# Kernel tuning notes

Measured on AMD Instinct MI355X. Metric: run time of the kernel, lower is better.

Reference implementation:

```python
import jax, jax.numpy as jnp
import numpy as np

N_NODES = 100000
N_EDGES = 1600000
IN_DIM = 128
HID = 32
HEADS = 4
NEG_SLOPE = 0.2


def gat_conv(x, src, dst, W, att_src, att_dst, bias, n_nodes, heads, out_ch):
    # x: [N, Fin], W: [Fin, heads*out_ch], att_*: [heads, out_ch], bias: [heads*out_ch]
    h = (x @ W).reshape(n_nodes, heads, out_ch)            # [N, H, C]
    a_src = jnp.einsum('nhc,hc->nh', h, att_src)           # [N, H]
    a_dst = jnp.einsum('nhc,hc->nh', h, att_dst)           # [N, H]
    e = jax.nn.leaky_relu(a_src[src] + a_dst[dst], NEG_SLOPE)  # [E, H]
    # segment softmax over incoming edges of each target node
    e_max = jax.ops.segment_max(e, dst, num_segments=n_nodes)  # [N, H]
    ex = jnp.exp(e - e_max[dst])                               # [E, H]
    denom = jax.ops.segment_sum(ex, dst, num_segments=n_nodes)  # [N, H]
    alpha = ex / denom[dst]                                     # [E, H]
    msg = h[src] * alpha[:, :, None]                            # [E, H, C]
    out = jax.ops.segment_sum(msg, dst, num_segments=n_nodes)   # [N, H, C]
    return out.reshape(n_nodes, heads * out_ch) + bias


def setup_inputs() -> dict:
    key = jax.random.key(0)
    ks = jax.random.split(key, 10)
    x = jax.random.normal(ks[0], (N_NODES, IN_DIM), dtype=jnp.float32)
    edge_index = jax.random.randint(ks[1], (2, N_EDGES), 0, N_NODES, dtype=jnp.int64) if jax.config.jax_enable_x64 else jax.random.randint(ks[1], (2, N_EDGES), 0, N_NODES, dtype=jnp.int32)
    s = 0.1
    W1 = jax.random.normal(ks[2], (IN_DIM, HEADS * HID), dtype=jnp.float32) * s
    att_src1 = jax.random.normal(ks[3], (HEADS, HID), dtype=jnp.float32) * s
    att_dst1 = jax.random.normal(ks[4], (HEADS, HID), dtype=jnp.float32) * s
    b1 = jnp.zeros((HEADS * HID,), dtype=jnp.float32)
    W2 = jax.random.normal(ks[5], (HEADS * HID, HEADS * HID), dtype=jnp.float32) * s
    att_src2 = jax.random.normal(ks[6], (HEADS, HID), dtype=jnp.float32) * s
    att_dst2 = jax.random.normal(ks[7], (HEADS, HID), dtype=jnp.float32) * s
    b2 = jnp.zeros((HEADS * HID,), dtype=jnp.float32)
    return {"x": x, "edge_index": edge_index, "W1": W1, "att_src1": att_src1,
            "att_dst1": att_dst1, "b1": b1, "W2": W2, "att_src2": att_src2,
            "att_dst2": att_dst2, "b2": b2}


def reference(x, edge_index, W1, att_src1, att_dst1, b1, W2, att_src2, att_dst2, b2):
    src, dst = edge_index[0], edge_index[1]
    x1 = jax.nn.relu(gat_conv(x, src, dst, W1, att_src1, att_dst1, b1, N_NODES, HEADS, HID))
    x2 = jax.nn.relu(gat_conv(x1, src, dst, W2, att_src2, att_dst2, b2, N_NODES, HEADS, HID))
    # [N, heads*hid, 2]
    return jnp.concatenate([x1[:, :, None], x2[:, :, None]], axis=2)
```

## Files before the change

### kernel.cpp

```cpp
#include <hip/hip_runtime.h>

#define NN 100000
#define NE 1600000
#define GEMM_GRID 1563
#define NBUK 391
#define BCAP 5120
#define PA_BLOCKS 320
#define PA_EDGES 5000
#define K1_GRID (16 + PA_BLOCKS)
#define K2_GRID (NBUK + GEMM_GRID)
#define AG1_GRID 6250
#define AGG2_GRID 12500

typedef short bf16x8 __attribute__((ext_vector_type(8)));
typedef float f32x4 __attribute__((ext_vector_type(4)));
typedef unsigned int u32;
typedef u32 u32x4 __attribute__((ext_vector_type(4)));
typedef unsigned short u16;

__device__ inline u32 bf16r(float x) {
    u32 u = __float_as_uint(x);
    return (u + 0x7FFFu + ((u >> 16) & 1u)) >> 16;
}

__device__ inline void split_pack8(const float a[8], u32 hh[4], u32 ll[4]) {
#pragma unroll
    for (int j = 0; j < 4; ++j) {
        u32 u0 = __float_as_uint(a[2 * j]);
        u32 u1 = __float_as_uint(a[2 * j + 1]);
        float l0 = a[2 * j] - __uint_as_float(u0 & 0xFFFF0000u);
        float l1 = a[2 * j + 1] - __uint_as_float(u1 & 0xFFFF0000u);
        hh[j] = (u0 >> 16) | (u1 & 0xFFFF0000u);
        ll[j] = (__float_as_uint(l0) >> 16) | (__float_as_uint(l1) & 0xFFFF0000u);
    }
}

__device__ inline void wpack_body(int idx, const float* __restrict__ W,
                                  bf16x8* __restrict__ wpH, bf16x8* __restrict__ wpL) {
    if (idx >= 2048) return;
    int lane = idx & 63, tile = idx >> 6;
    int kc = tile >> 3, ct = tile & 7;
    int col = lane & 15, kq = lane >> 4;
    int kbase = kc * 32 + kq * 8;
    float a[8];
#pragma unroll
    for (int i = 0; i < 8; ++i)
        a[i] = W[(size_t)(kbase + i) * 128 + ct * 16 + col];
    u32 hh[4], ll[4];
    split_pack8(a, hh, ll);
    wpH[tile * 64 + lane] = __builtin_bit_cast(bf16x8, (u32x4){hh[0], hh[1], hh[2], hh[3]});
    wpL[tile * 64 + lane] = __builtin_bit_cast(bf16x8, (u32x4){ll[0], ll[1], ll[2], ll[3]});
}

__global__ __launch_bounds__(256) void k1(
    const float* __restrict__ W1, bf16x8* __restrict__ wpH1, bf16x8* __restrict__ wpL1,
    const float* __restrict__ W2, bf16x8* __restrict__ wpH2, bf16x8* __restrict__ wpL2,
    const int* __restrict__ dst, const int* __restrict__ src,
    int* __restrict__ gtail, u32* __restrict__ tmp) {
    const int b = blockIdx.x;
    if (b < 8) {
        wpack_body(b * 256 + threadIdx.x, W1, wpH1, wpL1);
        return;
    } else if (b < 16) {
        wpack_body((b - 8) * 256 + threadIdx.x, W2, wpH2, wpL2);
        return;
    }
    __shared__ int lhist[NBUK], lcur[NBUK];
    const int t = threadIdx.x;
    const int e0 = (b - 16) * PA_EDGES;
    const int e1 = e0 + PA_EDGES;
    for (int i = t; i < NBUK; i += 256) lhist[i] = 0;
    __syncthreads();
    for (int e = e0 + t; e < e1; e += 256)
        atomicAdd(&lhist[dst[e] >> 8], 1);
    __syncthreads();
    for (int i = t; i < NBUK; i += 256)
        if (lhist[i] > 0) lcur[i] = atomicAdd(&gtail[i], lhist[i]);
    __syncthreads();
    for (int e = e0 + t; e < e1; e += 256) {
        int d = dst[e];
        int bb = d >> 8;
        int p = atomicAdd(&lcur[bb], 1);
        tmp[(size_t)bb * BCAP + p] = ((u32)(d & 255) << 17) | (u32)src[e];
    }
}

__device__ inline void gemm_epilogue(f32x4 acc[8], int row0, int w, int col, int kq,
                                     const float* __restrict__ atts,
                                     const float* __restrict__ attd,
                                     u16* __restrict__ hb,
                                     float* __restrict__ a_src,
                                     float* __restrict__ a_dst) {
    float as0[4], as1[4], ad0[4], ad1[4];
#pragma unroll
    for (int q = 0; q < 4; ++q) {
        as0[q] = atts[q * 32 + col];
        as1[q] = atts[q * 32 + 16 + col];
        ad0[q] = attd[q * 32 + col];
        ad1[q] = attd[q * 32 + 16 + col];
    }
#pragma unroll
    for (int r = 0; r < 4; ++r) {
        int node = row0 + w * 16 + kq * 4 + r;
        float ps[4], pd[4];
#pragma unroll
        for (int q = 0; q < 4; ++q) {
            float d0 = acc[2 * q][r], d1 = acc[2 * q + 1][r];
            ps[q] = d0 * as0[q] + d1 * as1[q];
            pd[q] = d0 * ad0[q] + d1 * ad1[q];
        }
#pragma unroll
        for (int off = 1; off < 16; off <<= 1) {
#pragma unroll
            for (int q = 0; q < 4; ++q) {
                ps[q] += __shfl_xor(ps[q], off);
                pd[q] += __shfl_xor(pd[q], off);
            }
        }
        if (node < NN) {
#pragma unroll
            for (int ct = 0; ct < 8; ++ct)
                hb[(size_t)node * 128 + ct * 16 + col] = (u16)bf16r(acc[ct][r]);
            if (col < 4) {
                float vs = col == 0 ? ps[0] : col == 1 ? ps[1] : col == 2 ? ps[2] : ps[3];
                float vd = col == 0 ? pd[0] : col == 1 ? pd[1] : col == 2 ? pd[2] : pd[3];
                a_src[node * 4 + col] = vs;
                a_dst[node * 4 + col] = vd;
            }
        }
    }
}

__global__ __launch_bounds__(256) void k2(
    const float* __restrict__ x,
    const bf16x8* __restrict__ wpH, const bf16x8* __restrict__ wpL,
    const float* __restrict__ atts, const float* __restrict__ attd,
    u16* __restrict__ hb, float* __restrict__ a_src, float* __restrict__ a_dst,
    const int* __restrict__ gtail, const u32* __restrict__ tmp,
    int* __restrict__ row_ptr, int* __restrict__ src_sorted) {
    __shared__ u32 ldata[BCAP];
    __shared__ int lh[256];
    __shared__ int lsc[256];
    const int idx = blockIdx.x;
    const int t = threadIdx.x;
    if (idx < NBUK) {
        const int g = idx;
        const int n = gtail[g];
        int acc = 0;
        for (int i = t; i < g; i += 256) acc += gtail[i];
        lsc[t] = acc;
        __syncthreads();
        for (int off = 128; off > 0; off >>= 1) {
            if (t < off) lsc[t] += lsc[t + off];
            __syncthreads();
        }
        const int ebase = lsc[0];
        lh[t] = 0;
        __syncthreads();
        for (int i = t; i < n; i += 256) {
            u32 v = tmp[(size_t)g * BCAP + i];
            ldata[i] = v;
            atomicAdd(&lh[v >> 17], 1);
        }
        __syncthreads();
        int c = lh[t];
        lsc[t] = c;
        __syncthreads();
        for (int off = 1; off < 256; off <<= 1) {
            int xv = (t >= off) ? lsc[t - off] : 0;
            __syncthreads();
            lsc[t] += xv;
            __syncthreads();
        }
        int excl = (t == 0) ? 0 : lsc[t - 1];
        int base = ebase + excl;
        lh[t] = base;
        int node = (g << 8) + t;
        if (node < NN) row_ptr[node] = base;
        if (g == NBUK - 1 && t == 0) row_ptr[NN] = ebase + n;
        __syncthreads();
        for (int i = t; i < n; i += 256) {
            u32 v = ldata[i];
            int p = atomicAdd(&lh[v >> 17], 1);
            src_sorted[p] = (int)(v & 0x1FFFFu);
        }
        return;
    }
    const int row0 = (idx - NBUK) * 64;
    const int lane = t & 63;
    const int w = t >> 6;
    const int col = lane & 15, kq = lane >> 4;
    int node_a = row0 + w * 16 + col;
    if (node_a > NN - 1) node_a = NN - 1;
    const float* xrow = x + (size_t)node_a * 128 + kq * 8;
    float a[32];
#pragma unroll
    for (int kc = 0; kc < 4; ++kc) {
        *(float4*)&a[kc * 8 + 0] = *(const float4*)(xrow + kc * 32);
        *(float4*)&a[kc * 8 + 4] = *(const float4*)(xrow + kc * 32 + 4);
    }
    f32x4 acc[8];
#pragma unroll
    for (int ct = 0; ct < 8; ++ct) acc[ct] = (f32x4){0.f, 0.f, 0.f, 0.f};
#pragma unroll
    for (int kc = 0; kc < 4; ++kc) {
        u32 hh[4], ll[4];
        split_pack8(&a[kc * 8], hh, ll);
        bf16x8 ah = __builtin_bit_cast(bf16x8, (u32x4){hh[0], hh[1], hh[2], hh[3]});
        bf16x8 al = __builtin_bit_cast(bf16x8, (u32x4){ll[0], ll[1], ll[2], ll[3]});
#pragma unroll
        for (int ct = 0; ct < 8; ++ct) {
            bf16x8 bh = wpH[(kc * 8 + ct) * 64 + lane];
            bf16x8 bl = wpL[(kc * 8 + ct) * 64 + lane];
            acc[ct] = __builtin_amdgcn_mfma_f32_16x16x32_bf16(ah, bh, acc[ct], 0, 0, 0);
            acc[ct] = __builtin_amdgcn_mfma_f32_16x16x32_bf16(al, bh, acc[ct], 0, 0, 0);
            acc[ct] = __builtin_amdgcn_mfma_f32_16x16x32_bf16(ah, bl, acc[ct], 0, 0, 0);
        }
    }
    gemm_epilogue(acc, row0, w, col, kq, atts, attd, hb, a_src, a_dst);
}

__global__ __launch_bounds__(256) void k_ag1(
    const u32* __restrict__ hb,
    const float* __restrict__ a_src, const float* __restrict__ a_dst,
    const int* __restrict__ row_ptr, const int* __restrict__ src_sorted,
    const float* __restrict__ bias1,
    const bf16x8* __restrict__ wpH2, const bf16x8* __restrict__ wpL2,
    const float* __restrict__ atts2, const float* __restrict__ attd2,
    u32* __restrict__ x1b, u16* __restrict__ hb2,
    float* __restrict__ a_src2, float* __restrict__ a_dst2) {
    __shared__ __align__(16) u32 xs[4][16][68];
    const int t = threadIdx.x;
    const int lane = t & 63;
    const int wv = t >> 6;
    const int q = lane >> 4;
    const int es = lane & 15;
    const int hbase = lane & 48;
    const int node0 = blockIdx.x * 16 + wv * 4;
    const float bv0 = bias1[lane * 2], bv1 = bias1[lane * 2 + 1];
#pragma unroll 1
    for (int ni = 0; ni < 4; ++ni) {
        const int node = node0 + ni;
        const int e0 = row_ptr[node], e1 = row_ptr[node + 1];
        const int emax = e1 - 1;
        const float advh = a_dst[node * 4 + q];
        float den = 0.f, a0a = 0.f, a0b = 0.f, a1a = 0.f, a1b = 0.f;
        if (e1 > e0) {
            int eidx = e0 + es;
            if (eidx > emax) eidx = emax;
            int sv = src_sorted[eidx];
            float av = a_src[sv * 4 + q];
            for (int ec = e0; ec < e1; ec += 16) {
                int cnt = e1 - ec;
                cnt = cnt < 16 ? cnt : 16;
                int eidxn = ec + 16 + es;
                if (eidxn > emax) eidxn = emax;
                int svn = src_sorted[eidxn];
                float avn = a_src[svn * 4 + q];
                float lk = av + advh;
                lk = lk > 0.f ? lk : 0.2f * lk;
                float ex = (es < cnt) ? __expf(lk - 8.f) : 0.f;
                den += ex;
                if (cnt == 16) {
                    u32 wvv[16];
#pragma unroll
                    for (int u = 0; u < 16; ++u) {
                        int su = __builtin_amdgcn_readlane(sv, u);
                        wvv[u] = hb[((size_t)su << 6) + lane];
                    }
                    float exu[16];
#pragma unroll
                    for (int u = 0; u < 16; ++u) exu[u] = __shfl(ex, hbase | u);
#pragma unroll
                    for (int u = 0; u < 16; ++u) {
                        float h0 = __uint_as_float(wvv[u] << 16);
                        float h1 = __uint_as_float(wvv[u] & 0xFFFF0000u);
                        if (u & 1) { a0b = fmaf(exu[u], h0, a0b); a1b = fmaf(exu[u], h1, a1b); }
                        else       { a0a = fmaf(exu[u], h0, a0a); a1a = fmaf(exu[u], h1, a1a); }
                    }
                } else {
                    for (int u0 = 0; u0 < cnt; u0 += 4) {
                        u32 wvv[4];
                        float exu[4];
#pragma unroll
                        for (int j = 0; j < 4; ++j) {
                            int su = __builtin_amdgcn_readlane(sv, u0 + j);
                            wvv[j] = hb[((size_t)su << 6) + lane];
                        }
#pragma unroll
                        for (int j = 0; j < 4; ++j) exu[j] = __shfl(ex, hbase | (u0 + j));
#pragma unroll
                        for (int j = 0; j < 4; ++j) {
                            float h0 = __uint_as_float(wvv[j] << 16);
                            float h1 = __uint_as_float(wvv[j] & 0xFFFF0000u);
                            if (j & 1) { a0b = fmaf(exu[j], h0, a0b); a1b = fmaf(exu[j], h1, a1b); }
                            else       { a0a = fmaf(exu[j], h0, a0a); a1a = fmaf(exu[j], h1, a1a); }
                        }
                    }
                }
                sv = svn;
                av = avn;
            }
        }
        float a0 = a0a + a0b, a1 = a1a + a1b;
#pragma unroll
        for (int m = 1; m < 16; m <<= 1) den += __shfl_xor(den, m);
        float inv = den > 0.f ? 1.f / den : 0.f;
        float r0 = fmaxf(fmaf(a0, inv, bv0), 0.f);
        float r1 = fmaxf(fmaf(a1, inv, bv1), 0.f);
        u32 pair = bf16r(r0) | (bf16r(r1) << 16);
        x1b[node * 64 + lane] = pair;
        xs[wv][ni][lane] = pair;
    }
    asm volatile("s_waitcnt lgkmcnt(0)" ::: "memory");
    __builtin_amdgcn_sched_barrier(0);
    const int col = lane & 15, kq = lane >> 4;
    int4 aw[4];
#pragma unroll
    for (int kc = 0; kc < 4; ++kc)
        aw[kc] = *(const int4*)&xs[wv][col & 3][kc * 16 + kq * 4];
    f32x4 acc[8];
#pragma unroll
    for (int ct = 0; ct < 8; ++ct) acc[ct] = (f32x4){0.f, 0.f, 0.f, 0.f};
#pragma unroll
    for (int kc = 0; kc < 4; ++kc) {
        bf16x8 a = __builtin_bit_cast(bf16x8, aw[kc]);
#pragma unroll
        for (int ct = 0; ct < 8; ++ct) {
            acc[ct] = __builtin_amdgcn_mfma_f32_16x16x32_bf16(a, wpH2[(kc * 8 + ct) * 64 + lane], acc[ct], 0, 0, 0);
            acc[ct] = __builtin_amdgcn_mfma_f32_16x16x32_bf16(a, wpL2[(kc * 8 + ct) * 64 + lane], acc[ct], 0, 0, 0);
        }
    }
    float as0[4], as1[4], ad0[4], ad1[4];
#pragma unroll
    for (int qq = 0; qq < 4; ++qq) {
        as0[qq] = atts2[qq * 32 + col];
        as1[qq] = atts2[qq * 32 + 16 + col];
        ad0[qq] = attd2[qq * 32 + col];
        ad1[qq] = attd2[qq * 32 + 16 + col];
    }
#pragma unroll
    for (int r = 0; r < 4; ++r) {
        int node = node0 + r;
        float ps[4], pd[4];
#pragma unroll
        for (int qq = 0; qq < 4; ++qq) {
            float d0 = acc[2 * qq][r], d1 = acc[2 * qq + 1][r];
            ps[qq] = d0 * as0[qq] + d1 * as1[qq];
            pd[qq] = d0 * ad0[qq] + d1 * ad1[qq];
        }
#pragma unroll
        for (int off = 1; off < 16; off <<= 1) {
#pragma unroll
            for (int qq = 0; qq < 4; ++qq) {
                ps[qq] += __shfl_xor(ps[qq], off);
                pd[qq] += __shfl_xor(pd[qq], off);
            }
        }
        if (kq == 0) {
#pragma unroll
            for (int ct = 0; ct < 8; ++ct)
                hb2[(size_t)node * 128 + ct * 16 + col] = (u16)bf16r(acc[ct][r]);
            if (col < 4) {
                float vs = col == 0 ? ps[0] : col == 1 ? ps[1] : col == 2 ? ps[2] : ps[3];
                float vd = col == 0 ? pd[0] : col == 1 ? pd[1] : col == 2 ? pd[2] : pd[3];
                a_src2[node * 4 + col] = vs;
                a_dst2[node * 4 + col] = vd;
            }
        }
    }
}

__global__ __launch_bounds__(256, 4) void k_agg2(
    const u32* __restrict__ hb,
    const float* __restrict__ a_src, const float* __restrict__ a_dst,
    const int* __restrict__ row_ptr, const int* __restrict__ src_sorted,
    const float* __restrict__ bias,
    const u32* __restrict__ x1b, float* __restrict__ outp) {
    const int lane = threadIdx.x & 63;
    const int node0 = blockIdx.x * 8 + (threadIdx.x >> 6) * 2;
    const int q = lane >> 4;
    const int es = lane & 15;
    const int hbase = lane & 48;
#pragma unroll
    for (int ni = 0; ni < 2; ++ni) {
        const int node = node0 + ni;
        if (node >= NN) continue;
        const int e0 = row_ptr[node], e1 = row_ptr[node + 1];
        const int emax = e1 - 1;
        const float advh = a_dst[node * 4 + q];
        float den = 0.f, a0a = 0.f, a0b = 0.f, a1a = 0.f, a1b = 0.f;
        if (e1 > e0) {
            int eidx = e0 + es;
            if (eidx > emax) eidx = emax;
            int sv = src_sorted[eidx];
            float av = a_src[sv * 4 + q];
            for (int ec = e0; ec < e1; ec += 16) {
                int cnt = e1 - ec;
                cnt = cnt < 16 ? cnt : 16;
                int eidxn = ec + 16 + es;
                if (eidxn > emax) eidxn = emax;
                int svn = src_sorted[eidxn];
                float avn = a_src[svn * 4 + q];
                float lk = av + advh;
                lk = lk > 0.f ? lk : 0.2f * lk;
                float ex = (es < cnt) ? __expf(lk - 8.f) : 0.f;
                den += ex;
                if (cnt == 16) {
                    u32 wv[16];
#pragma unroll
                    for (int u = 0; u < 16; ++u) {
                        int su = __builtin_amdgcn_readlane(sv, u);
                        wv[u] = hb[((size_t)su << 6) + lane];
                    }
                    float exu[16];
#pragma unroll
                    for (int u = 0; u < 16; ++u) exu[u] = __shfl(ex, hbase | u);
#pragma unroll
                    for (int u = 0; u < 16; ++u) {
                        float h0 = __uint_as_float(wv[u] << 16);
                        float h1 = __uint_as_float(wv[u] & 0xFFFF0000u);
                        if (u & 1) { a0b = fmaf(exu[u], h0, a0b); a1b = fmaf(exu[u], h1, a1b); }
                        else       { a0a = fmaf(exu[u], h0, a0a); a1a = fmaf(exu[u], h1, a1a); }
                    }
                } else {
                    for (int u0 = 0; u0 < cnt; u0 += 4) {
                        u32 wv[4];
                        float exu[4];
#pragma unroll
                        for (int j = 0; j < 4; ++j) {
                            int su = __builtin_amdgcn_readlane(sv, u0 + j);
                            wv[j] = hb[((size_t)su << 6) + lane];
                        }
#pragma unroll
                        for (int j = 0; j < 4; ++j) exu[j] = __shfl(ex, hbase | (u0 + j));
#pragma unroll
                        for (int j = 0; j < 4; ++j) {
                            float h0 = __uint_as_float(wv[j] << 16);
                            float h1 = __uint_as_float(wv[j] & 0xFFFF0000u);
                            if (j & 1) { a0b = fmaf(exu[j], h0, a0b); a1b = fmaf(exu[j], h1, a1b); }
                            else       { a0a = fmaf(exu[j], h0, a0a); a1a = fmaf(exu[j], h1, a1a); }
                        }
                    }
                }
                sv = svn;
                av = avn;
            }
        }
        float a0 = a0a + a0b, a1 = a1a + a1b;
#pragma unroll
        for (int m = 1; m < 16; m <<= 1) den += __shfl_xor(den, m);
        float inv = den > 0.f ? 1.f / den : 0.f;
        int c0 = lane * 2;
        float r0 = fmaxf(fmaf(a0, inv, bias[c0]), 0.f);
        float r1 = fmaxf(fmaf(a1, inv, bias[c0 + 1]), 0.f);
        u32 w1 = x1b[node * 64 + lane];
        float4 o;
        o.x = __uint_as_float(w1 << 16);
        o.y = r0;
        o.z = __uint_as_float(w1 & 0xFFFF0000u);
        o.w = r1;
        u32x4 ov = __builtin_bit_cast(u32x4, o);
        __builtin_nontemporal_store(ov,
            (u32x4*)(outp + (size_t)node * 256 + lane * 4));
    }
}


extern "C" void kernel_launch(void* const* d_in, const int* in_sizes, int n_in,
                              void* d_out, int out_size, void* d_ws, size_t ws_size,
                              hipStream_t stream) {
    const float* x   = (const float*)d_in[0];
    const int*   ei  = (const int*)d_in[1];
    const float* W1  = (const float*)d_in[2];
    const float* as1 = (const float*)d_in[3];
    const float* ad1 = (const float*)d_in[4];
    const float* b1  = (const float*)d_in[5];
    const float* W2  = (const float*)d_in[6];
    const float* as2 = (const float*)d_in[7];
    const float* ad2 = (const float*)d_in[8];
    const float* b2  = (const float*)d_in[9];
    float* out = (float*)d_out;
    const int* src = ei;
    const int* dst = ei + NE;

    char* w = (char*)d_ws;
    size_t off = 0;
    auto alloc = [&](size_t bytes) -> void* {
        void* p = w + off;
        off = (off + bytes + 255) & ~((size_t)255);
        return p;
    };
    u16* hb         = (u16*)alloc((size_t)NN * 128 * 2);
    u16* hb2        = (u16*)alloc((size_t)NN * 128 * 2);
    u32* x1b        = (u32*)alloc((size_t)NN * 64 * 4);
    float* a_src    = (float*)alloc((size_t)NN * 4 * 4);
    float* a_dst    = (float*)alloc((size_t)NN * 4 * 4);
    float* a_src2   = (float*)alloc((size_t)NN * 4 * 4);
    float* a_dst2   = (float*)alloc((size_t)NN * 4 * 4);
    int* row_ptr    = (int*)alloc((size_t)(NN + 1) * 4);
    int* gtail      = (int*)alloc(NBUK * 4);
    u32* tmp        = (u32*)alloc((size_t)NBUK * BCAP * 4);
    int* src_sorted = (int*)alloc((size_t)NE * 4);
    bf16x8* wpH1    = (bf16x8*)alloc(2048 * 16);
    bf16x8* wpL1    = (bf16x8*)alloc(2048 * 16);
    bf16x8* wpH2    = (bf16x8*)alloc(2048 * 16);
    bf16x8* wpL2    = (bf16x8*)alloc(2048 * 16);

    (void)hipMemsetAsync(gtail, 0, NBUK * 4, stream);
    k1<<<K1_GRID, 256, 0, stream>>>(W1, wpH1, wpL1, W2, wpH2, wpL2,
                                    dst, src, gtail, tmp);
    k2<<<K2_GRID, 256, 0, stream>>>(x, wpH1, wpL1, as1, ad1, hb, a_src, a_dst,
                                    gtail, tmp, row_ptr, src_sorted);
    k_ag1<<<AG1_GRID, 256, 0, stream>>>((const u32*)hb, a_src, a_dst, row_ptr,
                                        src_sorted, b1, wpH2, wpL2, as2, ad2,
                                        x1b, hb2, a_src2, a_dst2);
    k_agg2<<<AGG2_GRID, 256, 0, stream>>>((const u32*)hb2, a_src2, a_dst2,
                                          row_ptr, src_sorted, b2,
                                          (const u32*)x1b, out);
}
```

Measured before the change: 307.7 us.

## Share layer-2 GEMM tile across two waves in k_ag1 with 128-thread blocks

k_ag1 now runs 128-thread blocks of two waves that together aggregate 8 nodes and then share an 8-row tile in LDS for the layer-2 projection. Each wave computes half of the output column tiles (4 of 8), so the MFMA work per wave is halved. In the old code each wave padded a 4-node tile up to 16 rows and computed all 8 column tiles. This removes redundant MFMA and weight loads, at the cost of a block-wide __syncthreads and twice as many smaller blocks.

```diff
diff --git a/kernel.cpp b/kernel.cpp
--- a/kernel.cpp
+++ b/kernel.cpp
@@ -9,7 +9,7 @@
 #define PA_EDGES 5000
 #define K1_GRID (16 + PA_BLOCKS)
 #define K2_GRID (NBUK + GEMM_GRID)
-#define AG1_GRID 6250
+#define AG1_GRID 12500
 #define AGG2_GRID 12500
 
 typedef short bf16x8 __attribute__((ext_vector_type(8)));
@@ -220,7 +220,7 @@
     gemm_epilogue(acc, row0, w, col, kq, atts, attd, hb, a_src, a_dst);
 }
 
-__global__ __launch_bounds__(256) void k_ag1(
+__global__ __launch_bounds__(128) void k_ag1(
     const u32* __restrict__ hb,
     const float* __restrict__ a_src, const float* __restrict__ a_dst,
     const int* __restrict__ row_ptr, const int* __restrict__ src_sorted,
@@ -229,18 +229,18 @@
     const float* __restrict__ atts2, const float* __restrict__ attd2,
     u32* __restrict__ x1b, u16* __restrict__ hb2,
     float* __restrict__ a_src2, float* __restrict__ a_dst2) {
-    __shared__ __align__(16) u32 xs[4][16][68];
+    __shared__ __align__(16) u32 xs[8][68];
     const int t = threadIdx.x;
     const int lane = t & 63;
     const int wv = t >> 6;
     const int q = lane >> 4;
     const int es = lane & 15;
     const int hbase = lane & 48;
-    const int node0 = blockIdx.x * 16 + wv * 4;
+    const int node0 = blockIdx.x * 8;
     const float bv0 = bias1[lane * 2], bv1 = bias1[lane * 2 + 1];
 #pragma unroll 1
     for (int ni = 0; ni < 4; ++ni) {
-        const int node = node0 + ni;
+        const int node = node0 + wv * 4 + ni;
         const int e0 = row_ptr[node], e1 = row_ptr[node + 1];
         const int emax = e1 - 1;
         const float advh = a_dst[node * 4 + q];
@@ -310,41 +310,43 @@
         float r1 = fmaxf(fmaf(a1, inv, bv1), 0.f);
         u32 pair = bf16r(r0) | (bf16r(r1) << 16);
         x1b[node * 64 + lane] = pair;
-        xs[wv][ni][lane] = pair;
-    }
-    asm volatile("s_waitcnt lgkmcnt(0)" ::: "memory");
-    __builtin_amdgcn_sched_barrier(0);
+        xs[wv * 4 + ni][lane] = pair;
+    }
+    __syncthreads();
     const int col = lane & 15, kq = lane >> 4;
     int4 aw[4];
 #pragma unroll
     for (int kc = 0; kc < 4; ++kc)
-        aw[kc] = *(const int4*)&xs[wv][col & 3][kc * 16 + kq * 4];
-    f32x4 acc[8];
-#pragma unroll
-    for (int ct = 0; ct < 8; ++ct) acc[ct] = (f32x4){0.f, 0.f, 0.f, 0.f};
+        aw[kc] = *(const int4*)&xs[col & 7][kc * 16 + kq * 4];
+    f32x4 acc[4];
+#pragma unroll
+    for (int c = 0; c < 4; ++c) acc[c] = (f32x4){0.f, 0.f, 0.f, 0.f};
 #pragma unroll
     for (int kc = 0; kc < 4; ++kc) {
         bf16x8 a = __builtin_bit_cast(bf16x8, aw[kc]);
 #pragma unroll
-        for (int ct = 0; ct < 8; ++ct) {
-            acc[ct] = __builtin_amdgcn_mfma_f32_16x16x32_bf16(a, wpH2[(kc * 8 + ct) * 64 + lane], acc[ct], 0, 0, 0);
-            acc[ct] = __builtin_amdgcn_mfma_f32_16x16x32_bf16(a, wpL2[(kc * 8 + ct) * 64 + lane], acc[ct], 0, 0, 0);
-        }
-    }
-    float as0[4], as1[4], ad0[4], ad1[4];
-#pragma unroll
-    for (int qq = 0; qq < 4; ++qq) {
-        as0[qq] = atts2[qq * 32 + col];
-        as1[qq] = atts2[qq * 32 + 16 + col];
-        ad0[qq] = attd2[qq * 32 + col];
-        ad1[qq] = attd2[qq * 32 + 16 + col];
+        for (int c = 0; c < 4; ++c) {
+            int ct = wv * 4 + c;
+            acc[c] = __builtin_amdgcn_mfma_f32_16x16x32_bf16(a, wpH2[(kc * 8 + ct) * 64 + lane], acc[c], 0, 0, 0);
+            acc[c] = __builtin_amdgcn_mfma_f32_16x16x32_bf16(a, wpL2[(kc * 8 + ct) * 64 + lane], acc[c], 0, 0, 0);
+        }
+    }
+    float as0[2], as1[2], ad0[2], ad1[2];
+#pragma unroll
+    for (int qq = 0; qq < 2; ++qq) {
+        int hq = 2 * wv + qq;
+        as0[qq] = atts2[hq * 32 + col];
+        as1[qq] = atts2[hq * 32 + 16 + col];
+        ad0[qq] = attd2[hq * 32 + col];
+        ad1[qq] = attd2[hq * 32 + 16 + col];
     }
 #pragma unroll
     for (int r = 0; r < 4; ++r) {
-        int node = node0 + r;
-        float ps[4], pd[4];
-#pragma unroll
-        for (int qq = 0; qq < 4; ++qq) {
+        int rr = kq * 4 + r;
+        int node = node0 + rr;
+        float ps[2], pd[2];
+#pragma unroll
+        for (int qq = 0; qq < 2; ++qq) {
             float d0 = acc[2 * qq][r], d1 = acc[2 * qq + 1][r];
             ps[qq] = d0 * as0[qq] + d1 * as1[qq];
             pd[qq] = d0 * ad0[qq] + d1 * ad1[qq];
@@ -352,20 +354,19 @@
 #pragma unroll
         for (int off = 1; off < 16; off <<= 1) {
 #pragma unroll
-            for (int qq = 0; qq < 4; ++qq) {
+            for (int qq = 0; qq < 2; ++qq) {
                 ps[qq] += __shfl_xor(ps[qq], off);
                 pd[qq] += __shfl_xor(pd[qq], off);
             }
         }
-        if (kq == 0) {
-#pragma unroll
-            for (int ct = 0; ct < 8; ++ct)
-                hb2[(size_t)node * 128 + ct * 16 + col] = (u16)bf16r(acc[ct][r]);
-            if (col < 4) {
-                float vs = col == 0 ? ps[0] : col == 1 ? ps[1] : col == 2 ? ps[2] : ps[3];
-                float vd = col == 0 ? pd[0] : col == 1 ? pd[1] : col == 2 ? pd[2] : pd[3];
-                a_src2[node * 4 + col] = vs;
-                a_dst2[node * 4 + col] = vd;
+        if (kq < 2) {
+#pragma unroll
+            for (int c = 0; c < 4; ++c)
+                hb2[(size_t)node * 128 + (wv * 4 + c) * 16 + col] = (u16)bf16r(acc[c][r]);
+            if (col < 2) {
+                int hq = 2 * wv + col;
+                a_src2[node * 4 + hq] = col == 0 ? ps[0] : ps[1];
+                a_dst2[node * 4 + hq] = col == 0 ? pd[0] : pd[1];
             }
         }
     }
@@ -512,7 +513,7 @@
                                     dst, src, gtail, tmp);
     k2<<<K2_GRID, 256, 0, stream>>>(x, wpH1, wpL1, as1, ad1, hb, a_src, a_dst,
                                     gtail, tmp, row_ptr, src_sorted);
-    k_ag1<<<AG1_GRID, 256, 0, stream>>>((const u32*)hb, a_src, a_dst, row_ptr,
+    k_ag1<<<AG1_GRID, 128, 0, stream>>>((const u32*)hb, a_src, a_dst, row_ptr,
                                         src_sorted, b1, wpH2, wpL2, as2, ad2,
                                         x1b, hb2, a_src2, a_dst2);
     k_agg2<<<AGG2_GRID, 256, 0, stream>>>((const u32*)hb2, a_src2, a_dst2,
```

Measured after the change: 267.1 us. 13.2% less time.
